# Performance work log

Hardware: AMD Instinct MI355X
Metric: run time of the kernel (lower is better)

## Reference

```python
import jax, jax.numpy as jnp
import numpy as np

B, M, H, E, V, U = 1024, 15, 256, 256, 30000, 1000


def setup_inputs() -> dict:
    key = jax.random.key(0)
    ks = jax.random.split(key, 24)
    s = 0.05  # weight init scale
    return {
        "input_ids": jax.random.randint(ks[0], (B, 1), 0, V),
        "input_embedding": jax.random.normal(ks[1], (B, 1, E), jnp.float32),
        "hidden": jax.random.normal(ks[2], (1, B, H), jnp.float32),
        "inter_output": jax.random.normal(ks[3], (B, M, H), jnp.float32),
        "user_list": jax.random.randint(ks[4], (B,), 0, U),
        # per-user parameter tables (torch ModuleLists of Linear); stored [in,out]
        "inter_W": jax.random.normal(ks[5], (U, H, H), jnp.float32) * s,
        "inter_b": jax.random.normal(ks[6], (U, H), jnp.float32) * s,
        "hidden_W": jax.random.normal(ks[7], (U, H, H), jnp.float32) * s,
        "hidden_b": jax.random.normal(ks[8], (U, H), jnp.float32) * s,
        "lt1_W": jax.random.normal(ks[9], (U, 2 * H, H), jnp.float32) * s,
        "lt1_b": jax.random.normal(ks[10], (U, H), jnp.float32) * s,
        "scale_W": jax.random.normal(ks[11], (U, H), jnp.float32) * s,
        "scale_b": jax.random.normal(ks[12], (U,), jnp.float32) * s,
        # GRU (1 layer), torch layout: W_ih [3H, 2E], W_hh [3H, H], gate order r,z,n
        "gru_Wih": jax.random.normal(ks[13], (3 * H, 2 * E), jnp.float32) * s,
        "gru_Whh": jax.random.normal(ks[14], (3 * H, H), jnp.float32) * s,
        "gru_bih": jax.random.normal(ks[15], (3 * H,), jnp.float32) * s,
        "gru_bhh": jax.random.normal(ks[16], (3 * H,), jnp.float32) * s,
        # output projection, stored [H, V]
        "lin_W": jax.random.normal(ks[17], (H, V), jnp.float32) * s,
        "lin_b": jax.random.normal(ks[18], (V,), jnp.float32) * s,
    }


def reference(input_ids, input_embedding, hidden, inter_output, user_list,
              inter_W, inter_b, hidden_W, hidden_b, lt1_W, lt1_b,
              scale_W, scale_b, gru_Wih, gru_Whh, gru_bih, gru_bhh,
              lin_W, lin_b):
    embedded_input = input_embedding  # dropout p=0 (eval)
    hidden_t = jnp.transpose(hidden, (1, 0, 2))  # [B,1,H]

    # per-user intra attention: gather user weights, batched GEMMs (replaces python loop)
    Wi = inter_W[user_list]                      # [B,H,H]
    inter_output_a = jnp.einsum('bmh,bho->bmo', inter_output, Wi) + inter_b[user_list][:, None, :]
    Wh = hidden_W[user_list]                     # [B,H,H]
    hidden_t_a = jnp.einsum('bih,bho->bio', hidden_t, Wh) + hidden_b[user_list][:, None, :]  # [B,1,H]
    cat = jnp.concatenate([jnp.broadcast_to(hidden_t_a, (hidden_t_a.shape[0], M, H)), inter_output_a], axis=2)  # [B,M,2H]
    result = jnp.tanh(jnp.einsum('bmk,bko->bmo', cat, lt1_W[user_list]) + lt1_b[user_list][:, None, :])  # [B,M,H]
    energies = jnp.einsum('bmh,bh->bm', result, scale_W[user_list]) + scale_b[user_list][:, None]  # [B,M]

    attn_weights = jax.nn.softmax(energies, axis=1)                      # [B,M]
    context = jnp.einsum('bm,bmh->bh', attn_weights, inter_output)[:, None, :]  # [B,1,H]

    gru_input = jnp.concatenate([embedded_input, context], axis=2)  # [B,1,2E]
    x = gru_input[:, 0, :]
    h = hidden[0]
    gi = x @ gru_Wih.T + gru_bih   # [B,3H]
    gh = h @ gru_Whh.T + gru_bhh
    gi_r, gi_z, gi_n = jnp.split(gi, 3, axis=1)
    gh_r, gh_z, gh_n = jnp.split(gh, 3, axis=1)
    r = jax.nn.sigmoid(gi_r + gh_r)
    z = jax.nn.sigmoid(gi_z + gh_z)
    n = jnp.tanh(gi_n + r * gh_n)
    h_new = (1.0 - z) * n + z * h
    gru_output = h_new[:, None, :]       # [B,1,H]
    hidden_new = h_new[None, :, :]       # [1,B,H]

    output = gru_output @ lin_W + lin_b  # [B,1,V]
    return (output, hidden_new, embedded_input, gru_output, attn_weights)
```

## Files before the change

kernel.cpp:

```cpp
#include <hip/hip_runtime.h>
#include <math.h>

#define B 1024
#define M 15
#define H 256
#define E 256
#define V 30000
#define U 1000

typedef float  vf4    __attribute__((ext_vector_type(4)));
typedef __bf16 bf16x8 __attribute__((ext_vector_type(8)));
typedef float  f32x4  __attribute__((ext_vector_type(4)));

#define O_OUT   0
#define O_HID   ((size_t)B*V)
#define O_EMB   (O_HID + (size_t)B*H)
#define O_GRU   (O_EMB + (size_t)B*E)
#define O_ATT   (O_GRU + (size_t)B*H)

#define GLDS(g, l) __builtin_amdgcn_global_load_lds( \
    (const __attribute__((address_space(1))) void*)(g), \
    (__attribute__((address_space(3))) void*)(l), 16, 0, 0)

union BF8 { __bf16 h[8]; bf16x8 v; };
union BF4 { __bf16 h[4]; unsigned long long u; };

__global__ __launch_bounds__(1024) void sort_kernel(
    const int* __restrict__ ul, int* __restrict__ order, int* __restrict__ rbase_g)
{
    __shared__ int cnt[1024];
    __shared__ int base[1024];
    const int tid = threadIdx.x;
    cnt[tid] = 0;
    __syncthreads();
    const int u = ul[tid];
    atomicAdd(&cnt[u], 1);
    __syncthreads();
    int c0 = cnt[tid];
    int v  = c0;
    for (int off = 1; off < 1024; off <<= 1) {
        int add = (tid >= off) ? cnt[tid - off] : 0;
        __syncthreads();
        v += add;
        cnt[tid] = v;
        __syncthreads();
    }
    base[tid]   = v - c0;
    rbase_g[tid] = v - c0;
    __syncthreads();
    int pos = atomicAdd(&base[u], 1);
    order[pos] = tid;
}

#define FB_ATTN 1024
#define FB_TR   500
#define FB_WC   256
#define FB_TOT  (FB_ATTN + FB_TR + FB_WC)

__global__ __launch_bounds__(256, 4) void fused_pre_kernel(
    const float* __restrict__ hidden,
    const float* __restrict__ inter_output,
    const int*   __restrict__ user_list,
    const int*   __restrict__ order,
    const int*   __restrict__ rbase,
    const float* __restrict__ inter_W,
    const float* __restrict__ inter_b,
    const float* __restrict__ hidden_W,
    const float* __restrict__ hidden_b,
    const float* __restrict__ lt1_W,
    const float* __restrict__ lt1_b,
    const float* __restrict__ scale_W,
    const float* __restrict__ scale_b,
    const float* __restrict__ emb,
    const float* __restrict__ Wih,
    const float* __restrict__ Whh,
    const float* __restrict__ lin_W,
    float* __restrict__ out,
    __bf16* __restrict__ xcat,
    __bf16* __restrict__ wcat,
    __bf16* __restrict__ WT)
{
    __shared__ __align__(16) char smem[34432];
    const int bid = blockIdx.x;
    const int tid = threadIdx.x;

    if (bid >= FB_ATTN + FB_TR) {
        const int wb   = bid - (FB_ATTN + FB_TR);
        const int wave = tid >> 6, lane = tid & 63;
        const int n    = wb * 4 + wave;
        #pragma unroll
        for (int i = 0; i < 3; ++i) {
            int k = i * 256 + lane * 4;
            vf4 v = {0.f, 0.f, 0.f, 0.f};
            if (n < 512) {
                v = (k < 512) ? *(const vf4*)&Wih[(size_t)n * 512 + k]
                              : *(const vf4*)&Whh[(size_t)n * 256 + (k - 512)];
            } else if (n < 768) {
                if (k < 512) v = *(const vf4*)&Wih[(size_t)n * 512 + k];
            } else {
                if (k >= 512) v = *(const vf4*)&Whh[(size_t)(n - 256) * 256 + (k - 512)];
            }
            BF4 p;
            p.h[0]=(__bf16)v[0]; p.h[1]=(__bf16)v[1]; p.h[2]=(__bf16)v[2]; p.h[3]=(__bf16)v[3];
            *(unsigned long long*)&wcat[(size_t)n * 768 + k] = p.u;
        }
        return;
    }

    if (bid >= FB_ATTN) {
        const int t   = bid - FB_ATTN;
        const int v0  = (t % 125) * 240;
        const int k0  = (t / 125) * 64;
        const int lane = tid & 63, kq = tid >> 6;
        __bf16* T = (__bf16*)smem;

        if (lane < 60) {
            #pragma unroll
            for (int i = 0; i < 4; ++i) {
                int kr = kq * 16 + i * 4;
                vf4 f0 = *(const vf4*)&lin_W[(size_t)(k0 + kr + 0) * V + v0 + lane * 4];
                vf4 f1 = *(const vf4*)&lin_W[(size_t)(k0 + kr + 1) * V + v0 + lane * 4];
                vf4 f2 = *(const vf4*)&lin_W[(size_t)(k0 + kr + 2) * V + v0 + lane * 4];
                vf4 f3 = *(const vf4*)&lin_W[(size_t)(k0 + kr + 3) * V + v0 + lane * 4];
                #pragma unroll
                for (int j = 0; j < 4; ++j) {
                    BF4 pk;
                    pk.h[0] = (__bf16)f0[j];
                    pk.h[1] = (__bf16)f1[j];
                    pk.h[2] = (__bf16)f2[j];
                    pk.h[3] = (__bf16)f3[j];
                    int v = lane * 4 + j;
                    *(unsigned long long*)&T[v * 68 + kr] = pk.u;
                }
            }
        }
        __syncthreads();
        for (int r = 0; r < 15; ++r) {
            int L = r * 256 + tid;
            int v = L >> 4, c = L & 15;
            *(unsigned long long*)&WT[(size_t)(v0 + v) * H + k0 + c * 4] =
                *(const unsigned long long*)&T[v * 68 + c * 4];
        }
        return;
    }

    const int s   = ((bid & 7) << 7) + (bid >> 3);
    const int b0  = order[s];
    const int u   = user_list[b0];

    {
        float ev = emb[(size_t)b0 * E + tid];
        float hv = hidden[(size_t)b0 * H + tid];
        xcat[(size_t)b0 * 768 + tid]       = (__bf16)ev;
        xcat[(size_t)b0 * 768 + 512 + tid] = (__bf16)hv;
        out[O_EMB + (size_t)b0 * E + tid]  = ev;
    }

    if ((s - rbase[u]) & 1) return;
    bool paired = false;
    int  b1 = b0;
    if (s + 1 < B) {
        int ob = order[s + 1];
        if (user_list[ob] == u) { paired = true; b1 = ob; }
    }

    const int lane = tid & 63;
    const int wave = tid >> 6;
    const int wn0  = wave * 64;

    __bf16* Abuf = (__bf16*)smem;
    __bf16* hta  = (__bf16*)(smem + 32768);
    float*  red  = (float*)(smem + 32768 + 1024);
    float*  e_lds= (float*)(smem + 32768 + 1024 + 512);

    {
        const int r    = tid >> 3;
        const int part = tid & 7;
        const int sm   = r >> 4;
        const int mr   = r & 15;
        const int bs   = sm ? b1 : b0;
        const bool zr  = (sm == 1) && !paired;
        #pragma unroll
        for (int it = 0; it < 8; ++it) {
            int c = part + it * 8;
            int k = c * 8;
            BF8 p;
            #pragma unroll
            for (int j = 0; j < 8; ++j) p.h[j] = (__bf16)0.f;
            if (!zr) {
                if (mr < 15 && k < 256) {
                    vf4 f0 = *(const vf4*)&inter_output[(size_t)bs * M * H + mr * H + k];
                    vf4 f1 = *(const vf4*)&inter_output[(size_t)bs * M * H + mr * H + k + 4];
                    p.h[0]=(__bf16)f0[0]; p.h[1]=(__bf16)f0[1]; p.h[2]=(__bf16)f0[2]; p.h[3]=(__bf16)f0[3];
                    p.h[4]=(__bf16)f1[0]; p.h[5]=(__bf16)f1[1]; p.h[6]=(__bf16)f1[2]; p.h[7]=(__bf16)f1[3];
                } else if (mr == 15 && k >= 256) {
                    vf4 f0 = *(const vf4*)&hidden[(size_t)bs * H + (k - 256)];
                    vf4 f1 = *(const vf4*)&hidden[(size_t)bs * H + (k - 256) + 4];
                    p.h[0]=(__bf16)f0[0]; p.h[1]=(__bf16)f0[1]; p.h[2]=(__bf16)f0[2]; p.h[3]=(__bf16)f0[3];
                    p.h[4]=(__bf16)f1[0]; p.h[5]=(__bf16)f1[1]; p.h[6]=(__bf16)f1[2]; p.h[7]=(__bf16)f1[3];
                }
            }
            *(bf16x8*)&Abuf[r * 512 + (c ^ (r & 7)) * 8] = p.v;
        }
    }
    __syncthreads();

    const float* Wi_base  = inter_W  + (size_t)u * H * H;
    const float* Wh_base  = hidden_W + (size_t)u * H * H;
    const float* lt1_base = lt1_W    + (size_t)u * 2 * H * H;

    const int ocol = wn0 + (lane & 15);
    const int krow = (lane >> 4) * 8;

    f32x4 acc1[2][4];
    #pragma unroll
    for (int mf = 0; mf < 2; ++mf)
        #pragma unroll
        for (int nf = 0; nf < 4; ++nf) { f32x4 z = {0.f,0.f,0.f,0.f}; acc1[mf][nf] = z; }

    #pragma unroll 2
    for (int ks = 0; ks < 16; ++ks) {
        const float* Bp = ((ks < 8) ? (Wi_base + (size_t)(ks * 32) * H)
                                    : (Wh_base + (size_t)((ks - 8) * 32) * H))
                          + (size_t)krow * H + ocol;
        float t[4][8];
        #pragma unroll
        for (int j = 0; j < 8; ++j)
            #pragma unroll
            for (int nf = 0; nf < 4; ++nf)
                t[nf][j] = Bp[(size_t)j * H + nf * 16];
        bf16x8 bfr[4];
        #pragma unroll
        for (int nf = 0; nf < 4; ++nf) {
            BF8 pk;
            #pragma unroll
            for (int j = 0; j < 8; ++j) pk.h[j] = (__bf16)t[nf][j];
            bfr[nf] = pk.v;
        }
        int sca = ((ks * 4 + (lane >> 4)) ^ (lane & 7)) * 8;
        bf16x8 a0 = *(const bf16x8*)&Abuf[(lane & 15) * 512 + sca];
        #pragma unroll
        for (int nf = 0; nf < 4; ++nf)
            acc1[0][nf] = __builtin_amdgcn_mfma_f32_16x16x32_bf16(a0, bfr[nf], acc1[0][nf], 0, 0, 0);
        if (paired) {
            bf16x8 a1 = *(const bf16x8*)&Abuf[(16 + (lane & 15)) * 512 + sca];
            #pragma unroll
            for (int nf = 0; nf < 4; ++nf)
                acc1[1][nf] = __builtin_amdgcn_mfma_f32_16x16x32_bf16(a1, bfr[nf], acc1[1][nf], 0, 0, 0);
        }
    }
    __syncthreads();

    if ((lane >> 4) == 3) {
        #pragma unroll
        for (int nf = 0; nf < 4; ++nf) {
            int o = wn0 + nf * 16 + (lane & 15);
            float hb = hidden_b[(size_t)u * H + o];
            hta[o]       = (__bf16)(acc1[0][nf][3] + hb);
            hta[256 + o] = (__bf16)(acc1[1][nf][3] + hb);
        }
    }
    #pragma unroll
    for (int mf = 0; mf < 2; ++mf) {
        #pragma unroll
        for (int nf = 0; nf < 4; ++nf) {
            int o  = wn0 + nf * 16 + (lane & 15);
            float bi = inter_b[(size_t)u * H + o];
            int k  = 256 + o;
            #pragma unroll
            for (int j = 0; j < 4; ++j) {
                int r  = mf * 16 + (lane >> 4) * 4 + j;
                Abuf[r * 512 + ((k >> 3) ^ (r & 7)) * 8 + (k & 7)] = (__bf16)(acc1[mf][nf][j] + bi);
            }
        }
    }
    __syncthreads();

    {
        const int r    = tid >> 3;
        const int part = tid & 7;
        const int sm   = r >> 4;
        #pragma unroll
        for (int it = 0; it < 4; ++it) {
            int c = part + it * 8;
            bf16x8 hv = *(const bf16x8*)&hta[sm * 256 + c * 8];
            *(bf16x8*)&Abuf[r * 512 + (c ^ (r & 7)) * 8] = hv;
        }
    }
    __syncthreads();

    f32x4 acc2[2][4];
    #pragma unroll
    for (int mf = 0; mf < 2; ++mf)
        #pragma unroll
        for (int nf = 0; nf < 4; ++nf) { f32x4 z = {0.f,0.f,0.f,0.f}; acc2[mf][nf] = z; }

    #pragma unroll 2
    for (int ks = 0; ks < 16; ++ks) {
        const float* Bp = lt1_base + (size_t)(ks * 32) * H + (size_t)krow * H + ocol;
        float t[4][8];
        #pragma unroll
        for (int j = 0; j < 8; ++j)
            #pragma unroll
            for (int nf = 0; nf < 4; ++nf)
                t[nf][j] = Bp[(size_t)j * H + nf * 16];
        bf16x8 bfr[4];
        #pragma unroll
        for (int nf = 0; nf < 4; ++nf) {
            BF8 pk;
            #pragma unroll
            for (int j = 0; j < 8; ++j) pk.h[j] = (__bf16)t[nf][j];
            bfr[nf] = pk.v;
        }
        int sca = ((ks * 4 + (lane >> 4)) ^ (lane & 7)) * 8;
        bf16x8 a0 = *(const bf16x8*)&Abuf[(lane & 15) * 512 + sca];
        #pragma unroll
        for (int nf = 0; nf < 4; ++nf)
            acc2[0][nf] = __builtin_amdgcn_mfma_f32_16x16x32_bf16(a0, bfr[nf], acc2[0][nf], 0, 0, 0);
        if (paired) {
            bf16x8 a1 = *(const bf16x8*)&Abuf[(16 + (lane & 15)) * 512 + sca];
            #pragma unroll
            for (int nf = 0; nf < 4; ++nf)
                acc2[1][nf] = __builtin_amdgcn_mfma_f32_16x16x32_bf16(a1, bfr[nf], acc2[1][nf], 0, 0, 0);
        }
    }

    float p0[4] = {0.f,0.f,0.f,0.f};
    float p1[4] = {0.f,0.f,0.f,0.f};
    #pragma unroll
    for (int nf = 0; nf < 4; ++nf) {
        int o = wn0 + nf * 16 + (lane & 15);
        float l1b = lt1_b[(size_t)u * H + o];
        float sw  = scale_W[(size_t)u * H + o];
        #pragma unroll
        for (int j = 0; j < 4; ++j)
            p0[j] += tanhf(acc2[0][nf][j] + l1b) * sw;
        if (paired)
            #pragma unroll
            for (int j = 0; j < 4; ++j)
                p1[j] += tanhf(acc2[1][nf][j] + l1b) * sw;
    }
    #pragma unroll
    for (int j = 0; j < 4; ++j) {
        float v = p0[j];
        v += __shfl_xor(v, 1, 64); v += __shfl_xor(v, 2, 64);
        v += __shfl_xor(v, 4, 64); v += __shfl_xor(v, 8, 64);
        if ((lane & 15) == 0) red[0 * 64 + wave * 16 + (lane >> 4) * 4 + j] = v;
        float w = p1[j];
        w += __shfl_xor(w, 1, 64); w += __shfl_xor(w, 2, 64);
        w += __shfl_xor(w, 4, 64); w += __shfl_xor(w, 8, 64);
        if ((lane & 15) == 0) red[1 * 64 + wave * 16 + (lane >> 4) * 4 + j] = w;
    }
    __syncthreads();
    if (tid < 32) {
        int sm = tid >> 4, mm = tid & 15;
        e_lds[sm * 16 + mm] = red[sm * 64 + mm] + red[sm * 64 + 16 + mm]
                            + red[sm * 64 + 32 + mm] + red[sm * 64 + 48 + mm]
                            + scale_b[u];
    }
    __syncthreads();

    const int nsm = paired ? 2 : 1;
    for (int sm = 0; sm < nsm; ++sm) {
        const int bs = sm ? b1 : b0;
        float mx = -1e30f;
        #pragma unroll
        for (int m = 0; m < M; ++m) mx = fmaxf(mx, e_lds[sm * 16 + m]);
        float sum = 0.f;
        float aw[M];
        #pragma unroll
        for (int m = 0; m < M; ++m) { aw[m] = expf(e_lds[sm * 16 + m] - mx); sum += aw[m]; }
        float inv = 1.f / sum;
        if (tid < M) out[O_ATT + (size_t)bs * M + tid] = aw[tid] * inv;
        float ctx = 0.f;
        #pragma unroll
        for (int m = 0; m < M; ++m)
            ctx += aw[m] * inter_output[(size_t)bs * M * H + m * H + tid];
        xcat[(size_t)bs * 768 + 256 + tid] = (__bf16)(ctx * inv);
    }
}

__global__ __launch_bounds__(256) void xgemm_kernel(
    const __bf16* __restrict__ xcat, const __bf16* __restrict__ wcat,
    float* __restrict__ gates)
{
    const int n0   = blockIdx.x * 64;
    const int m0   = blockIdx.y * 64;
    const int tid  = threadIdx.x;
    const int wave = tid >> 6, lane = tid & 63;
    const int wm   = wave >> 1, wn = wave & 1;

    __shared__ __align__(16) __bf16 Al[64 * 128];
    __shared__ __align__(16) __bf16 Bl[64 * 128];

    f32x4 acc[2][2];
    #pragma unroll
    for (int mf = 0; mf < 2; ++mf)
        #pragma unroll
        for (int nf = 0; nf < 2; ++nf) { f32x4 z = {0.f,0.f,0.f,0.f}; acc[mf][nf] = z; }

    for (int ks = 0; ks < 6; ++ks) {
        #pragma unroll
        for (int r = 0; r < 4; ++r) {
            int L = r * 256 + tid;
            int row = L >> 4, c = L & 15;
            int sc = c ^ (row & 7);
            GLDS(xcat + (size_t)(m0 + row) * 768 + ks * 128 + sc * 8, &Al[(size_t)L * 8]);
        }
        #pragma unroll
        for (int r = 0; r < 4; ++r) {
            int L = r * 256 + tid;
            int row = L >> 4, c = L & 15;
            int sc = c ^ (row & 7);
            GLDS(wcat + (size_t)(n0 + row) * 768 + ks * 128 + sc * 8, &Bl[(size_t)L * 8]);
        }
        __syncthreads();
        #pragma unroll
        for (int kk = 0; kk < 4; ++kk) {
            bf16x8 af[2];
            #pragma unroll
            for (int mf = 0; mf < 2; ++mf) {
                int row = wm * 32 + mf * 16 + (lane & 15);
                int c   = kk * 4 + (lane >> 4);
                af[mf] = *(const bf16x8*)&Al[row * 128 + (c ^ (row & 7)) * 8];
            }
            bf16x8 bfr[2];
            #pragma unroll
            for (int nf = 0; nf < 2; ++nf) {
                int col = wn * 32 + nf * 16 + (lane & 15);
                int c   = kk * 4 + (lane >> 4);
                bfr[nf] = *(const bf16x8*)&Bl[col * 128 + (c ^ (col & 7)) * 8];
            }
            #pragma unroll
            for (int mf = 0; mf < 2; ++mf)
                #pragma unroll
                for (int nf = 0; nf < 2; ++nf)
                    acc[mf][nf] = __builtin_amdgcn_mfma_f32_16x16x32_bf16(
                        af[mf], bfr[nf], acc[mf][nf], 0, 0, 0);
        }
        __syncthreads();
    }

    #pragma unroll
    for (int nf = 0; nf < 2; ++nf) {
        int n = n0 + wn * 32 + nf * 16 + (lane & 15);
        #pragma unroll
        for (int mf = 0; mf < 2; ++mf) {
            int rb = m0 + wm * 32 + mf * 16 + (lane >> 4) * 4;
            f32x4 a = acc[mf][nf];
            #pragma unroll
            for (int j = 0; j < 4; ++j)
                gates[(size_t)(rb + j) * 1024 + n] = a[j];
        }
    }
}

__global__ __launch_bounds__(256) void gate_kernel(
    const float* __restrict__ gates,
    const float* __restrict__ hidden,
    const float* __restrict__ bih, const float* __restrict__ bhh,
    float* __restrict__ out, __bf16* __restrict__ hnb)
{
    const int b = blockIdx.x, j = threadIdx.x;
    const float* g = gates + (size_t)b * 1024;
    float rs  = g[j]       + bih[j]       + bhh[j];
    float zs  = g[256 + j] + bih[256 + j] + bhh[256 + j];
    float gin = g[512 + j] + bih[512 + j];
    float ghn = g[768 + j] + bhh[512 + j];
    float h   = hidden[(size_t)b * H + j];
    float r_  = 1.f / (1.f + expf(-rs));
    float z_  = 1.f / (1.f + expf(-zs));
    float n_  = tanhf(gin + r_ * ghn);
    float hn  = (1.f - z_) * n_ + z_ * h;
    out[O_HID + (size_t)b * H + j] = hn;
    out[O_GRU + (size_t)b * H + j] = hn;
    hnb[(size_t)b * H + j] = (__bf16)hn;
}

#define GBM 64
#define GBN 256
#define GBK 64
#define NTM 16
#define NWG ((117 + 1) * NTM)
__global__ __launch_bounds__(256) void out_mfma_kernel(
    const __bf16* __restrict__ hnb,
    const __bf16* __restrict__ WT,
    const float* __restrict__ lin_b,
    float* __restrict__ out)
{
    const int L  = blockIdx.x;
    const int s  = (L & 7) * (NWG / 8) + (L >> 3);
    const int nt = s >> 4, mt = s & 15;
    const int n0 = nt * GBN;
    const int m0 = mt * GBM;
    const int tid  = threadIdx.x;
    const int wave = tid >> 6, lane = tid & 63;

    __shared__ __align__(16) char gsm[GBM * H * 2 + GBN * GBK * 2];
    __bf16* Al = (__bf16*)gsm;
    __bf16* Bl = (__bf16*)(gsm + GBM * H * 2);

    #pragma unroll
    for (int r = 0; r < 8; ++r) {
        int Li = r * 256 + tid;
        int m = Li >> 5;
        int c = Li & 31;
        int sc = c ^ (m & 7);
        GLDS(hnb + (size_t)(m0 + m) * H + sc * 8, &Al[(size_t)Li * 8]);
    }

    f32x4 acc[4][4];
    #pragma unroll
    for (int mf = 0; mf < 4; ++mf)
        #pragma unroll
        for (int nf = 0; nf < 4; ++nf) {
            f32x4 z = {0.f, 0.f, 0.f, 0.f};
            acc[mf][nf] = z;
        }

    const int wn0 = wave * 64;

    for (int ks = 0; ks < 4; ++ks) {
        #pragma unroll
        for (int r = 0; r < 8; ++r) {
            int Li = r * 256 + tid;
            int n = Li >> 3;
            int c = Li & 7;
            int sc = c ^ (n & 7);
            int nn = n0 + n; if (nn >= V) nn = V - 1;
            GLDS(WT + (size_t)nn * H + ks * GBK + sc * 8, &Bl[(size_t)Li * 8]);
        }
        __syncthreads();

        #pragma unroll
        for (int kk = 0; kk < 2; ++kk) {
            bf16x8 af[4];
            #pragma unroll
            for (int mf = 0; mf < 4; ++mf) {
                int row = mf * 16 + (lane & 15);
                int c   = ks * 8 + kk * 4 + (lane >> 4);
                int cs  = c ^ (row & 7);
                af[mf] = *(const bf16x8*)&Al[row * H + cs * 8];
            }
            bf16x8 bfr[4];
            #pragma unroll
            for (int nf = 0; nf < 4; ++nf) {
                int col = wn0 + nf * 16 + (lane & 15);
                int c   = kk * 4 + (lane >> 4);
                int cs  = c ^ (col & 7);
                bfr[nf] = *(const bf16x8*)&Bl[col * GBK + cs * 8];
            }
            #pragma unroll
            for (int mf = 0; mf < 4; ++mf)
                #pragma unroll
                for (int nf = 0; nf < 4; ++nf)
                    acc[mf][nf] = __builtin_amdgcn_mfma_f32_16x16x32_bf16(
                        af[mf], bfr[nf], acc[mf][nf], 0, 0, 0);
        }
        __syncthreads();
    }

    float* Cs = (float*)gsm;
    #pragma unroll
    for (int nf = 0; nf < 4; ++nf) {
        int col = wn0 + nf * 16 + (lane & 15);
        #pragma unroll
        for (int mf = 0; mf < 4; ++mf) {
            #pragma unroll
            for (int j = 0; j < 4; ++j)
                Cs[(mf * 16 + (lane >> 4) * 4 + j) * 256 + col] = acc[mf][nf][j];
        }
    }
    __syncthreads();

    const bool nok = (n0 + lane * 4 + 3 < V);
    f32x4 lb = {0.f, 0.f, 0.f, 0.f};
    if (nok) lb = *(const f32x4*)&lin_b[n0 + lane * 4];
    for (int r = wave; r < 64; r += 4) {
        f32x4 c = *(const f32x4*)&Cs[r * 256 + lane * 4];
        c += lb;
        if (nok)
            *(f32x4*)&out[(size_t)(m0 + r) * V + n0 + lane * 4] = c;
    }
}

extern "C" void kernel_launch(void* const* d_in, const int* in_sizes, int n_in,
                              void* d_out, int out_size, void* d_ws, size_t ws_size,
                              hipStream_t stream) {
    const float* emb    = (const float*)d_in[1];
    const float* hidden = (const float*)d_in[2];
    const float* io     = (const float*)d_in[3];
    const int*   ul     = (const int*)  d_in[4];
    const float* iW     = (const float*)d_in[5];
    const float* ib     = (const float*)d_in[6];
    const float* hW     = (const float*)d_in[7];
    const float* hb     = (const float*)d_in[8];
    const float* l1W    = (const float*)d_in[9];
    const float* l1b    = (const float*)d_in[10];
    const float* sW     = (const float*)d_in[11];
    const float* sb     = (const float*)d_in[12];
    const float* Wih    = (const float*)d_in[13];
    const float* Whh    = (const float*)d_in[14];
    const float* bih    = (const float*)d_in[15];
    const float* bhh    = (const float*)d_in[16];
    const float* lW     = (const float*)d_in[17];
    const float* lb     = (const float*)d_in[18];

    float* out = (float*)d_out;
    char* ws = (char*)d_ws;
    int*    order = (int*)ws;
    int*    rbase = (int*)(ws + 4096);
    __bf16* xcat  = (__bf16*)(ws + 8192);
    __bf16* wcat  = (__bf16*)(ws + 8192 + 1572864);
    float*  gates = (float*) (ws + 8192 + 2 * 1572864);
    __bf16* hnb   = (__bf16*)(ws + 8192 + 2 * 1572864 + 4194304);
    __bf16* WT    = (__bf16*)(ws + 8192 + 2 * 1572864 + 4194304 + 524288);

    sort_kernel<<<1, 1024, 0, stream>>>(ul, order, rbase);
    fused_pre_kernel<<<FB_TOT, 256, 0, stream>>>(
        hidden, io, ul, order, rbase, iW, ib, hW, hb, l1W, l1b, sW, sb,
        emb, Wih, Whh, lW, out, xcat, wcat, WT);
    xgemm_kernel<<<dim3(16, 16), 256, 0, stream>>>(xcat, wcat, gates);
    gate_kernel<<<B, 256, 0, stream>>>(gates, hidden, bih, bhh, out, hnb);
    out_mfma_kernel<<<NWG, 256, 0, stream>>>(hnb, WT, lb, out);
}
```

Baseline: 244.1 us.

## Fuse GRU gate epilogue into gate GEMM via interleaved weight rows

The packed GRU weight rows are permuted so that each group of four consecutive GEMM output columns holds the r, z, input-n and hidden-n gates of one hidden unit. The GEMM can then run the gate nonlinearities in its epilogue from a shared-memory staging tile. This removes the separate gate kernel, one launch, and the round trip of the 4 MB gates buffer through global memory. It also lowers the occupancy hint of the pre kernel from 4 to 3, at the cost of extra LDS in the GEMM and a smaller wave grid for the gate math.

```diff
diff --git a/kernel.cpp b/kernel.cpp
--- a/kernel.cpp
+++ b/kernel.cpp
@@ -57,7 +57,7 @@
 #define FB_WC   256
 #define FB_TOT  (FB_ATTN + FB_TR + FB_WC)
 
-__global__ __launch_bounds__(256, 4) void fused_pre_kernel(
+__global__ __launch_bounds__(256, 3) void fused_pre_kernel(
     const float* __restrict__ hidden,
     const float* __restrict__ inter_output,
     const int*   __restrict__ user_list,
@@ -88,17 +88,18 @@
         const int wb   = bid - (FB_ATTN + FB_TR);
         const int wave = tid >> 6, lane = tid & 63;
         const int n    = wb * 4 + wave;
+        const int r    = (n >> 2) + ((n & 3) << 8);
         #pragma unroll
         for (int i = 0; i < 3; ++i) {
             int k = i * 256 + lane * 4;
             vf4 v = {0.f, 0.f, 0.f, 0.f};
-            if (n < 512) {
-                v = (k < 512) ? *(const vf4*)&Wih[(size_t)n * 512 + k]
-                              : *(const vf4*)&Whh[(size_t)n * 256 + (k - 512)];
-            } else if (n < 768) {
-                if (k < 512) v = *(const vf4*)&Wih[(size_t)n * 512 + k];
+            if (r < 512) {
+                v = (k < 512) ? *(const vf4*)&Wih[(size_t)r * 512 + k]
+                              : *(const vf4*)&Whh[(size_t)r * 256 + (k - 512)];
+            } else if (r < 768) {
+                if (k < 512) v = *(const vf4*)&Wih[(size_t)r * 512 + k];
             } else {
-                if (k >= 512) v = *(const vf4*)&Whh[(size_t)(n - 256) * 256 + (k - 512)];
+                if (k >= 512) v = *(const vf4*)&Whh[(size_t)(r - 256) * 256 + (k - 512)];
             }
             BF4 p;
             p.h[0]=(__bf16)v[0]; p.h[1]=(__bf16)v[1]; p.h[2]=(__bf16)v[2]; p.h[3]=(__bf16)v[3];
@@ -380,9 +381,11 @@
     }
 }
 
-__global__ __launch_bounds__(256) void xgemm_kernel(
+__global__ __launch_bounds__(256) void xgemm_gate_kernel(
     const __bf16* __restrict__ xcat, const __bf16* __restrict__ wcat,
-    float* __restrict__ gates)
+    const float* __restrict__ hidden,
+    const float* __restrict__ bih, const float* __restrict__ bhh,
+    float* __restrict__ out, __bf16* __restrict__ hnb)
 {
     const int n0   = blockIdx.x * 64;
     const int m0   = blockIdx.y * 64;
@@ -392,6 +395,7 @@
 
     __shared__ __align__(16) __bf16 Al[64 * 128];
     __shared__ __align__(16) __bf16 Bl[64 * 128];
+    __shared__ __align__(16) float  Cs[64 * 68];
 
     f32x4 acc[2][2];
     #pragma unroll
@@ -443,38 +447,38 @@
 
     #pragma unroll
     for (int nf = 0; nf < 2; ++nf) {
-        int n = n0 + wn * 32 + nf * 16 + (lane & 15);
+        int lc = wn * 32 + nf * 16 + (lane & 15);
         #pragma unroll
         for (int mf = 0; mf < 2; ++mf) {
-            int rb = m0 + wm * 32 + mf * 16 + (lane >> 4) * 4;
+            int lr = wm * 32 + mf * 16 + (lane >> 4) * 4;
             f32x4 a = acc[mf][nf];
             #pragma unroll
             for (int j = 0; j < 4; ++j)
-                gates[(size_t)(rb + j) * 1024 + n] = a[j];
-        }
-    }
-}
-
-__global__ __launch_bounds__(256) void gate_kernel(
-    const float* __restrict__ gates,
-    const float* __restrict__ hidden,
-    const float* __restrict__ bih, const float* __restrict__ bhh,
-    float* __restrict__ out, __bf16* __restrict__ hnb)
-{
-    const int b = blockIdx.x, j = threadIdx.x;
-    const float* g = gates + (size_t)b * 1024;
-    float rs  = g[j]       + bih[j]       + bhh[j];
-    float zs  = g[256 + j] + bih[256 + j] + bhh[256 + j];
-    float gin = g[512 + j] + bih[512 + j];
-    float ghn = g[768 + j] + bhh[512 + j];
-    float h   = hidden[(size_t)b * H + j];
-    float r_  = 1.f / (1.f + expf(-rs));
-    float z_  = 1.f / (1.f + expf(-zs));
-    float n_  = tanhf(gin + r_ * ghn);
-    float hn  = (1.f - z_) * n_ + z_ * h;
-    out[O_HID + (size_t)b * H + j] = hn;
-    out[O_GRU + (size_t)b * H + j] = hn;
-    hnb[(size_t)b * H + j] = (__bf16)hn;
+                Cs[(lr + j) * 68 + lc] = a[j];
+        }
+    }
+    __syncthreads();
+
+    #pragma unroll
+    for (int k = 0; k < 4; ++k) {
+        int idx = k * 256 + tid;
+        int r = idx >> 4, g = idx & 15;
+        f32x4 c = *(const f32x4*)&Cs[r * 68 + g * 4];
+        int b = m0 + r;
+        int j = (n0 >> 2) + g;
+        float rs  = c[0] + bih[j]       + bhh[j];
+        float zs  = c[1] + bih[256 + j] + bhh[256 + j];
+        float gin = c[2] + bih[512 + j];
+        float ghn = c[3] + bhh[512 + j];
+        float h   = hidden[(size_t)b * H + j];
+        float r_  = 1.f / (1.f + expf(-rs));
+        float z_  = 1.f / (1.f + expf(-zs));
+        float n_  = tanhf(gin + r_ * ghn);
+        float hn  = (1.f - z_) * n_ + z_ * h;
+        out[O_HID + (size_t)b * H + j] = hn;
+        out[O_GRU + (size_t)b * H + j] = hn;
+        hnb[(size_t)b * H + j] = (__bf16)hn;
+    }
 }
 
 #define GBM 64
@@ -612,15 +616,13 @@
     int*    rbase = (int*)(ws + 4096);
     __bf16* xcat  = (__bf16*)(ws + 8192);
     __bf16* wcat  = (__bf16*)(ws + 8192 + 1572864);
-    float*  gates = (float*) (ws + 8192 + 2 * 1572864);
-    __bf16* hnb   = (__bf16*)(ws + 8192 + 2 * 1572864 + 4194304);
-    __bf16* WT    = (__bf16*)(ws + 8192 + 2 * 1572864 + 4194304 + 524288);
+    __bf16* hnb   = (__bf16*)(ws + 8192 + 2 * 1572864);
+    __bf16* WT    = (__bf16*)(ws + 8192 + 2 * 1572864 + 524288);
 
     sort_kernel<<<1, 1024, 0, stream>>>(ul, order, rbase);
     fused_pre_kernel<<<FB_TOT, 256, 0, stream>>>(
         hidden, io, ul, order, rbase, iW, ib, hW, hb, l1W, l1b, sW, sb,
         emb, Wih, Whh, lW, out, xcat, wcat, WT);
-    xgemm_kernel<<<dim3(16, 16), 256, 0, stream>>>(xcat, wcat, gates);
-    gate_kernel<<<B, 256, 0, stream>>>(gates, hidden, bih, bhh, out, hnb);
+    xgemm_gate_kernel<<<dim3(16, 16), 256, 0, stream>>>(xcat, wcat, hidden, bih, bhh, out, hnb);
     out_mfma_kernel<<<NWG, 256, 0, stream>>>(hnb, WT, lb, out);
 }
```

Measured after the change: 240.1 us. About the same (-1.6%).
